# Kernel optimization log

Hardware: AMD Instinct MI355X
Metric: run time of the kernel (lower is better)

Reference implementation:

```python
import jax, jax.numpy as jnp
import numpy as np

CHUNK = 32
H = 4

def silu(x):
    return x * jax.nn.sigmoid(x)

def l2norm(x):
    return x * jax.lax.rsqrt(jnp.sum(x * x, -1, keepdims=True) + 1e-6)

def dwconv_causal(x_cl, w):
    # x_cl: (b, C, L), w: (C, k) depthwise causal conv (cross-correlation, left pad k-1)
    k = w.shape[1]
    xp = jnp.pad(x_cl, ((0, 0), (0, 0), (k - 1, 0)))
    return jax.lax.conv_general_dilated(xp, w[:, None, :], (1,), 'VALID',
        dimension_numbers=('NCH', 'OIH', 'NCH'), feature_group_count=x_cl.shape[1])

def short_conv_silu(x_bld, w):
    y = dwconv_causal(jnp.swapaxes(x_bld, 1, 2), w)
    return silu(jnp.swapaxes(y, 1, 2))

def delta_rule_chunkwise(q, k, v, beta, chunk=CHUNK):
    # q,k: (b,h,L,dk)  v: (b,h,L,dv)  beta: (b,h,L)
    b, h, L, dk = q.shape
    dv = v.shape[-1]
    pad = (-L) % chunk
    if pad:
        q, k, v = (jnp.pad(t, ((0, 0), (0, 0), (0, pad), (0, 0))) for t in (q, k, v))
        beta = jnp.pad(beta, ((0, 0), (0, 0), (0, pad)))
    n = (L + pad) // chunk
    q = l2norm(q)
    k = l2norm(k)
    v = v * beta[..., None]
    kb = k * beta[..., None]
    ch = lambda x: x.reshape(b, h, n, chunk, x.shape[-1])
    qc, kc, vc, kbc = map(ch, (q, k, v, kb))
    idx = jnp.arange(chunk)
    strict_lower = (idx[:, None] > idx[None, :]).astype(q.dtype)
    incl_lower = (idx[:, None] >= idx[None, :]).astype(q.dtype)
    # forward substitution to invert (I - tril(beta K K^T, -1)) per chunk
    attn = -jnp.einsum('bhncd,bhned->bhnce', kbc, kc) * strict_lower
    for i in range(1, chunk):
        upd = jnp.einsum('...j,...ji->...i', attn[..., i, :], attn[..., :, :i])
        attn = attn.at[..., i, :i].add(upd)
    attn = attn + jnp.eye(chunk, dtype=q.dtype)
    u = attn @ vc          # (b,h,n,c,dv)
    w = attn @ kbc         # (b,h,n,c,dk)
    xs = tuple(jnp.moveaxis(t, 2, 0) for t in (qc, kc, u, w))
    S0 = jnp.zeros((b, h, dk, dv), q.dtype)
    def step(S, x):
        qi, ki, ui, wi = x
        a_loc = jnp.einsum('bhcd,bhed->bhce', qi, ki) * incl_lower
        ui = ui - wi @ S
        oi = qi @ S + a_loc @ ui
        S = S + jnp.einsum('bhcd,bhcv->bhdv', ki, ui)
        return S, oi
    S, o = jax.lax.scan(step, S0, xs)
    o = jnp.moveaxis(o, 0, 2).reshape(b, h, n * chunk, dv)[:, :, :L]
    return o, S

def multiscale_conv(v, ms_w3, ms_w15, ms_w31, kernel_mix_w, channel_mixer_w):
    # v: (b,l,h,d)
    b, l, h, d = v.shape
    x = jnp.swapaxes(v.reshape(b, l, h * d), 1, 2)  # (b, h*d, l)
    outs = [dwconv_causal(x, w) for w in (ms_w3, ms_w15, ms_w31)]
    y = jnp.concatenate(outs, axis=1)               # (b, 3*h*d, l)
    # faithful to torch rearrange 'b (h kd) l -> b l h kd' on the concat layout
    y = y.reshape(b, h, 3 * d, l).transpose(0, 3, 1, 2)  # (b,l,h,3d)
    y = y @ kernel_mix_w                            # (b,l,h,d)
    y = (y.reshape(b, l, h * d) @ channel_mixer_w).reshape(b, l, h, d)
    return y

def _forward(hidden_states, Wq, Wk, Wv, Wb, conv_q_w, conv_k_w, conv_v_w,
             ms_w3, ms_w15, ms_w31, kernel_mix_w, channel_mixer_w,
             fusion_w1, fusion_b1, fusion_w2, fusion_b2, o_norm_w, Wo):
    b, L, D = hidden_states.shape
    h = H
    dk = Wq.shape[1] // h
    dv = Wv.shape[1] // h
    q = short_conv_silu(hidden_states @ Wq, conv_q_w).reshape(b, L, h, dk)
    k = short_conv_silu(hidden_states @ Wk, conv_k_w).reshape(b, L, h, dk)
    v = short_conv_silu(hidden_states @ Wv, conv_v_w).reshape(b, L, h, dv)
    v_direct = v
    beta = jax.nn.sigmoid(hidden_states @ Wb)  # (b,L,h)
    tr = lambda x: jnp.swapaxes(x, 1, 2)
    delta_out, _S = delta_rule_chunkwise(tr(q), tr(k), tr(v), tr(beta))
    delta_out = jnp.swapaxes(delta_out, 1, 2)  # (b,L,h,dv)
    ms_out = multiscale_conv(v_direct, ms_w3, ms_w15, ms_w31, kernel_mix_w, channel_mixer_w)
    bn = lambda x: jnp.mean(jnp.abs(x), -1)    # (b,L,h)
    gate_features = jnp.concatenate([hidden_states, bn(ms_out), bn(delta_out), bn(v_direct)], -1)
    hdn = jax.nn.gelu(gate_features @ fusion_w1 + fusion_b1, approximate=False)
    logits = (hdn @ fusion_w2 + fusion_b2).reshape(b, L, h, 3)
    wts = jax.nn.softmax(logits, -1)
    o = wts[..., 0:1] * ms_out + wts[..., 1:2] * delta_out + wts[..., 2:3] * v_direct
    o = o * jax.lax.rsqrt(jnp.mean(o * o, -1, keepdims=True) + 1e-5) * o_norm_w  # RMSNorm
    return o.reshape(b, L, h * dv) @ Wo

def setup_inputs() -> dict:
    B, L, D = 4, 2048, 1024
    h, d = H, D // H
    key = jax.random.key(0)
    ks = jax.random.split(key, 20)
    nrm = lambda k, shp, s: (jax.random.normal(k, shp, dtype=jnp.float32) * s)
    inp = {
        'hidden_states': nrm(ks[0], (B, L, D), 1.0),
        'Wq': nrm(ks[1], (D, D), D ** -0.5),
        'Wk': nrm(ks[2], (D, D), D ** -0.5),
        'Wv': nrm(ks[3], (D, D), D ** -0.5),
        'Wb': nrm(ks[4], (D, h), D ** -0.5),
        'conv_q_w': nrm(ks[5], (D, 4), 0.3),
        'conv_k_w': nrm(ks[6], (D, 4), 0.3),
        'conv_v_w': nrm(ks[7], (D, 4), 0.3),
        'ms_w3': nrm(ks[8], (D, 3), 0.02),
        'ms_w15': nrm(ks[9], (D, 15), 0.02),
        'ms_w31': nrm(ks[10], (D, 31), 0.02),
        'kernel_mix_w': nrm(ks[11], (3 * d, d), (3 * d) ** -0.5),
        'channel_mixer_w': nrm(ks[12], (D, D), D ** -0.5),
        'fusion_w1': nrm(ks[13], (D + 3 * h, 2 * D), (D + 3 * h) ** -0.5),
        'fusion_b1': jnp.zeros((2 * D,), jnp.float32),
        'fusion_w2': nrm(ks[14], (2 * D, 3 * h), (2 * D) ** -0.5),
        'fusion_b2': jnp.concatenate([jnp.zeros((2 * h,), jnp.float32), jnp.ones((h,), jnp.float32)]),
        'o_norm_w': jnp.ones((d,), jnp.float32),
        'Wo': nrm(ks[15], (D, D), D ** -0.5),
    }
    return inp

def reference(hidden_states, Wq, Wk, Wv, Wb, conv_q_w, conv_k_w, conv_v_w,
              ms_w3, ms_w15, ms_w31, kernel_mix_w, channel_mixer_w,
              fusion_w1, fusion_b1, fusion_w2, fusion_b2, o_norm_w, Wo):
    return _forward(hidden_states, Wq, Wk, Wv, Wb, conv_q_w, conv_k_w, conv_v_w,
                    ms_w3, ms_w15, ms_w31, kernel_mix_w, channel_mixer_w,
                    fusion_w1, fusion_b1, fusion_w2, fusion_b2, o_norm_w, Wo)
```

## Files before the change

### kernel.cpp

```cpp
#include <hip/hip_runtime.h>
#include <math.h>


typedef __attribute__((ext_vector_type(8))) __bf16 bf16x8;
typedef __attribute__((ext_vector_type(4))) float f32x4;

__device__ inline ushort f2bf(float f) {
    union { float f; unsigned u; } x; x.f = f;
    unsigned u = x.u;
    u += 0x7fffu + ((u >> 16) & 1u);
    return (ushort)(u >> 16);
}
__device__ inline float bf2f(ushort h) {
    union { unsigned u; float f; } x; x.u = ((unsigned)h) << 16;
    return x.f;
}
__device__ inline float ldf(float v) { return v; }
__device__ inline float ldf(ushort v) { return bf2f(v); }

template<int EPI>
__global__ __launch_bounds__(256) void gemm_mfma(
    const ushort* __restrict__ A, const ushort* __restrict__ BT,
    const float* __restrict__ bias, const float* __restrict__ extA,
    const float* __restrict__ extB, void* __restrict__ Cout,
    int M, int N, int K)
{
    __shared__ ushort As[2][128 * 32];
    __shared__ ushort Bs[2][128 * 32];
    __shared__ float bns[(EPI >= 2) ? 128 * 13 : 1];
    __shared__ float exb[(EPI >= 2) ? 12 * 128 : 1];
    const int tid = threadIdx.x;
    const int nwg = gridDim.x * gridDim.y;
    int lin = blockIdx.y * gridDim.x + blockIdx.x;
    lin = (lin & 7) * (nwg >> 3) + (lin >> 3);
    const int row0 = (lin / gridDim.x) * 128, col0 = (lin % gridDim.x) * 128;
    const int lane = tid & 63, wave = tid >> 6;
    const int wr = (wave >> 1) * 64, wc = (wave & 1) * 64;

    if (EPI >= 2) {
        for (int e = tid; e < 128 * 12; e += 256)
            bns[(e / 12) * 13 + (e % 12)] = extA[(long)(row0 + e / 12) * 12 + e % 12];
        for (int e = tid; e < 12 * 128; e += 256)
            exb[e] = extB[(long)(e >> 7) * N + col0 + (e & 127)];
    }

    f32x4 acc[4][4];
    #pragma unroll
    for (int m = 0; m < 4; ++m)
        #pragma unroll
        for (int n = 0; n < 4; ++n) {
            acc[m][n][0] = 0.f; acc[m][n][1] = 0.f;
            acc[m][n][2] = 0.f; acc[m][n][3] = 0.f;
        }

    const int rA = lane & 15;
    const int ko = (lane >> 4) * 8;
    const int srow = tid >> 2;
    const int skk = (tid & 3) * 8;

    for (int k0 = 0; k0 < K; k0 += 64) {
        #pragma unroll
        for (int hf = 0; hf < 2; ++hf) {
            #pragma unroll
            for (int i = 0; i < 2; ++i) {
                const long ga = (long)(row0 + i * 64 + srow) * K + k0 + hf * 32 + skk;
                __builtin_amdgcn_global_load_lds(
                    (const __attribute__((address_space(1))) void*)(A + ga),
                    (__attribute__((address_space(3))) void*)(&As[hf][0] + i * 2048 + wave * 512),
                    16, 0, 0);
                const long gb = (long)(col0 + i * 64 + srow) * K + k0 + hf * 32 + skk;
                __builtin_amdgcn_global_load_lds(
                    (const __attribute__((address_space(1))) void*)(BT + gb),
                    (__attribute__((address_space(3))) void*)(&Bs[hf][0] + i * 2048 + wave * 512),
                    16, 0, 0);
            }
        }
        __syncthreads();
        #pragma unroll
        for (int hf = 0; hf < 2; ++hf) {
            bf16x8 af[4], bfr[4];
            #pragma unroll
            for (int m = 0; m < 4; ++m)
                af[m] = *(const bf16x8*)(&As[hf][0] + (wr + m * 16 + rA) * 32 + ko);
            #pragma unroll
            for (int n = 0; n < 4; ++n)
                bfr[n] = *(const bf16x8*)(&Bs[hf][0] + (wc + n * 16 + rA) * 32 + ko);
            #pragma unroll
            for (int m = 0; m < 4; ++m)
                #pragma unroll
                for (int n = 0; n < 4; ++n)
                    acc[m][n] = __builtin_amdgcn_mfma_f32_16x16x32_bf16(af[m], bfr[n], acc[m][n], 0, 0, 0);
        }
        __syncthreads();
    }

    const int crow = (lane >> 4) * 4;
    const int ccol = lane & 15;
    #pragma unroll
    for (int m = 0; m < 4; ++m) {
        #pragma unroll
        for (int n = 0; n < 4; ++n) {
            #pragma unroll
            for (int r = 0; r < 4; ++r) {
                const int rl = wr + m * 16 + crow + r;
                const int cl = wc + n * 16 + ccol;
                float vv = acc[m][n][r];
                if (EPI >= 2) {
                    vv += bias[col0 + cl];
                    #pragma unroll
                    for (int j = 0; j < 12; ++j) vv += bns[rl * 13 + j] * exb[j * 128 + cl];
                    vv = 0.5f * vv * (1.f + erff(vv * 0.70710678118654752f));
                }
                const long off = (long)(row0 + rl) * N + col0 + cl;
                if (EPI == 0) ((float*)Cout)[off] = vv;
                else ((ushort*)Cout)[off] = f2bf(vv);
            }
        }
    }
}

__global__ __launch_bounds__(256) void transpose_cast(const float* __restrict__ W,
    ushort* __restrict__ WT, int K, int N)
{
    __shared__ float t[32][33];
    const int k0 = blockIdx.y * 32, n0 = blockIdx.x * 32;
    const int c = threadIdx.x & 31, r8 = threadIdx.x >> 5;
    #pragma unroll
    for (int rr = 0; rr < 4; ++rr) {
        const int r = r8 + rr * 8;
        t[r][c] = W[(long)(k0 + r) * N + n0 + c];
    }
    __syncthreads();
    #pragma unroll
    for (int rr = 0; rr < 4; ++rr) {
        const int r = r8 + rr * 8;
        WT[(long)(n0 + r) * K + k0 + c] = f2bf(t[c][r]);
    }
}

__global__ __launch_bounds__(256) void cast_bf16(const float* __restrict__ x,
    ushort* __restrict__ y)
{
    const long i = ((long)blockIdx.x * 256 + threadIdx.x) * 4;
    const float4 v = *(const float4*)(x + i);
    ushort4 o;
    o.x = f2bf(v.x); o.y = f2bf(v.y); o.z = f2bf(v.z); o.w = f2bf(v.w);
    *(ushort4*)(y + i) = o;
}

template<int NOUT, int MODE, typename TA>
__global__ __launch_bounds__(256) void gemm_smallN(const TA* __restrict__ A,
    const float* __restrict__ Bm, const float* __restrict__ bias,
    float* __restrict__ Cm, int K)
{
    __shared__ float part[4][NOUT];
    __shared__ float sm[NOUT];
    const int m = blockIdx.x, tid = threadIdx.x;
    const TA* ar = A + (long)m * K;
    float acc[NOUT];
    #pragma unroll
    for (int j = 0; j < NOUT; ++j) acc[j] = 0.f;
    for (int k = tid; k < K; k += 256) {
        const float a = ldf(ar[k]);
        #pragma unroll
        for (int j = 0; j < NOUT; ++j) acc[j] += a * Bm[(long)k * NOUT + j];
    }
    #pragma unroll
    for (int j = 0; j < NOUT; ++j)
        for (int off = 32; off > 0; off >>= 1) acc[j] += __shfl_down(acc[j], off);
    const int wid = tid >> 6, lane = tid & 63;
    if (lane == 0) {
        #pragma unroll
        for (int j = 0; j < NOUT; ++j) part[wid][j] = acc[j];
    }
    __syncthreads();
    if (tid < NOUT) {
        float s = part[0][tid] + part[1][tid] + part[2][tid] + part[3][tid];
        if (MODE == 0) {
            Cm[(long)m * NOUT + tid] = 1.f / (1.f + expf(-s));
        } else {
            sm[tid] = s + bias[tid];
        }
    }
    if (MODE == 1) {
        __syncthreads();
        if (tid < NOUT) {
            const int hh = tid / 3, r = tid - hh * 3;
            const float a0 = sm[hh * 3], a1 = sm[hh * 3 + 1], a2 = sm[hh * 3 + 2];
            const float mx = fmaxf(a0, fmaxf(a1, a2));
            const float e0 = expf(a0 - mx), e1 = expf(a1 - mx), e2 = expf(a2 - mx);
            const float mine = (r == 0) ? e0 : ((r == 1) ? e1 : e2);
            Cm[(long)m * NOUT + tid] = mine / (e0 + e1 + e2);
        }
    }
}

__global__ __launch_bounds__(256) void conv4_silu(const float* __restrict__ x,
    int xstride, int coff, const float* __restrict__ wc, float* __restrict__ y)
{
    const long idx = (long)blockIdx.x * 256 + threadIdx.x;
    const int c = (int)(idx & 1023);
    const long bl = idx >> 10;
    const int l = (int)(bl & 2047);
    const float* xp = x + bl * xstride + coff + c;
    const float* wp = wc + c * 4;
    float s = 0.f;
    #pragma unroll
    for (int t = 0; t < 4; ++t) {
        const int ll = l - 3 + t;
        if (ll >= 0) s += xp[(long)(ll - l) * xstride] * wp[t];
    }
    y[idx] = s / (1.f + expf(-s));
}

__global__ __launch_bounds__(256) void conv4_silu_l2norm(const float* __restrict__ x,
    int xstride, int coff, const float* __restrict__ wc, ushort* __restrict__ y)
{
    const int bl = blockIdx.x, tid = threadIdx.x;
    const int l = bl & 2047;
    const int c0 = tid * 4;
    const float* xp = x + (long)bl * xstride + coff + c0;
    float s[4] = {0.f, 0.f, 0.f, 0.f};
    #pragma unroll
    for (int t = 0; t < 4; ++t) {
        const int ll = l - 3 + t;
        if (ll >= 0) {
            const float4 xv = *(const float4*)(xp + (long)(ll - l) * xstride);
            s[0] += xv.x * wc[(c0 + 0) * 4 + t];
            s[1] += xv.y * wc[(c0 + 1) * 4 + t];
            s[2] += xv.z * wc[(c0 + 2) * 4 + t];
            s[3] += xv.w * wc[(c0 + 3) * 4 + t];
        }
    }
    #pragma unroll
    for (int i = 0; i < 4; ++i) s[i] = s[i] / (1.f + expf(-s[i]));
    float ss = s[0] * s[0] + s[1] * s[1] + s[2] * s[2] + s[3] * s[3];
    for (int off = 32; off > 0; off >>= 1) ss += __shfl_down(ss, off);
    ss = __shfl(ss, 0);
    const float inv = rsqrtf(ss + 1e-6f);
    ushort4 o;
    o.x = f2bf(s[0] * inv); o.y = f2bf(s[1] * inv);
    o.z = f2bf(s[2] * inv); o.w = f2bf(s[3] * inv);
    *(ushort4*)(y + (long)bl * 1024 + c0) = o;
}

__global__ __launch_bounds__(256) void chunk_prep(
    const ushort* __restrict__ qn, const ushort* __restrict__ kn,
    const float* __restrict__ v, const float* __restrict__ beta,
    float* __restrict__ u, ushort* __restrict__ w16,
    ushort* __restrict__ kT16, ushort* __restrict__ al16)
{
    __shared__ __align__(16) ushort kn16[32 * 264];
    __shared__ __align__(16) ushort kb16[32 * 264];
    __shared__ __align__(16) float  vb[32 * 260];
    __shared__ float Ms[32 * 33];
    __shared__ float Rs[32 * 33];
    __shared__ float bet[32];
    const int blk = blockIdx.x;
    const int n = blk & 63;
    const int bh = blk >> 6;
    const int h = bh & 3;
    const int b = bh >> 2;
    const int tid = threadIdx.x;
    const long lbase = (long)b * 2048 + n * 32;

    if (tid < 32) bet[tid] = beta[(lbase + tid) * 4 + h];
    __syncthreads();

    #pragma unroll
    for (int it = 0; it < 4; ++it) {
        const int e2 = tid + it * 256;
        const int c = e2 >> 5, d8 = (e2 & 31) * 8;
        const uint4 kv = *(const uint4*)(kn + (lbase + c) * 1024 + h * 256 + d8);
        *(uint4*)&kn16[c * 264 + d8] = kv;
        const float bc = bet[c];
        uint4 kb;
        kb.x = (uint)f2bf(bf2f((ushort)(kv.x & 0xffffu)) * bc) |
               ((uint)f2bf(bf2f((ushort)(kv.x >> 16)) * bc) << 16);
        kb.y = (uint)f2bf(bf2f((ushort)(kv.y & 0xffffu)) * bc) |
               ((uint)f2bf(bf2f((ushort)(kv.y >> 16)) * bc) << 16);
        kb.z = (uint)f2bf(bf2f((ushort)(kv.z & 0xffffu)) * bc) |
               ((uint)f2bf(bf2f((ushort)(kv.z >> 16)) * bc) << 16);
        kb.w = (uint)f2bf(bf2f((ushort)(kv.w & 0xffffu)) * bc) |
               ((uint)f2bf(bf2f((ushort)(kv.w >> 16)) * bc) << 16);
        *(uint4*)&kb16[c * 264 + d8] = kb;
    }
    #pragma unroll
    for (int it = 0; it < 8; ++it) {
        const int e2 = tid + it * 256;
        const int c = e2 >> 6, d4 = (e2 & 63) * 4;
        float4 vv = *(const float4*)(v + (lbase + c) * 1024 + h * 256 + d4);
        const float bc = bet[c];
        vv.x *= bc; vv.y *= bc; vv.z *= bc; vv.w *= bc;
        *(float4*)&vb[c * 260 + d4] = vv;
    }
    __syncthreads();

    for (int e = tid; e < 8192; e += 256)
        kT16[(long)blk * 8192 + e] = kn16[(e & 31) * 264 + (e >> 5)];

    const int lane = tid & 63, wave = tid >> 6;
    const int wr2 = (wave >> 1) * 16, wc2 = (wave & 1) * 16;
    const int rA = lane & 15, ko = (lane >> 4) * 8;
    {
        f32x4 accM, accA;
        accM[0] = 0.f; accM[1] = 0.f; accM[2] = 0.f; accM[3] = 0.f;
        accA[0] = 0.f; accA[1] = 0.f; accA[2] = 0.f; accA[3] = 0.f;
        const ushort* qrow = qn + (lbase + wr2 + rA) * 1024 + h * 256 + ko;
        #pragma unroll
        for (int ks = 0; ks < 8; ++ks) {
            const bf16x8 bfK = *(const bf16x8*)&kn16[(wc2 + rA) * 264 + ks * 32 + ko];
            const bf16x8 afM = *(const bf16x8*)&kb16[(wr2 + rA) * 264 + ks * 32 + ko];
            accM = __builtin_amdgcn_mfma_f32_16x16x32_bf16(afM, bfK, accM, 0, 0, 0);
            const bf16x8 afQ = *(const bf16x8*)(qrow + ks * 32);
            accA = __builtin_amdgcn_mfma_f32_16x16x32_bf16(afQ, bfK, accA, 0, 0, 0);
        }
        const int ccol = lane & 15, crow = (lane >> 4) * 4;
        #pragma unroll
        for (int r = 0; r < 4; ++r) {
            const int i = wr2 + crow + r, j = wc2 + ccol;
            const float mv = (i > j) ? -accM[r] : 0.f;
            Ms[i * 33 + j] = mv;
            Rs[i * 33 + j] = mv + ((i == j) ? 1.f : 0.f);
            al16[(long)blk * 1024 + i * 32 + j] = f2bf((i >= j) ? accA[r] : 0.f);
        }
    }
    __syncthreads();

    const int j = tid & 31, i0 = tid >> 5;
    for (int it = 0; it < 4; ++it) {
        float p4[4] = {0.f, 0.f, 0.f, 0.f};
        for (int kk = 0; kk < 32; ++kk) {
            const float pb = Ms[kk * 33 + j];
            #pragma unroll
            for (int ii = 0; ii < 4; ++ii) p4[ii] += Ms[(i0 + 8 * ii) * 33 + kk] * pb;
        }
        __syncthreads();
        #pragma unroll
        for (int ii = 0; ii < 4; ++ii) Ms[(i0 + 8 * ii) * 33 + j] = p4[ii];
        __syncthreads();
        float r4[4] = {0.f, 0.f, 0.f, 0.f};
        for (int kk = 0; kk < 32; ++kk) {
            const float pb = Ms[kk * 33 + j];
            #pragma unroll
            for (int ii = 0; ii < 4; ++ii) r4[ii] += Rs[(i0 + 8 * ii) * 33 + kk] * pb;
        }
        __syncthreads();
        #pragma unroll
        for (int ii = 0; ii < 4; ++ii) Rs[(i0 + 8 * ii) * 33 + j] += r4[ii];
        __syncthreads();
    }

    {
        const int dd = tid;
        float accU[32], accW[32];
        #pragma unroll
        for (int r = 0; r < 32; ++r) { accU[r] = 0.f; accW[r] = 0.f; }
        for (int kk = 0; kk < 32; ++kk) {
            const float vv = vb[kk * 260 + dd];
            const float bb = bf2f(kb16[kk * 264 + dd]);
            #pragma unroll
            for (int r = 0; r < 32; ++r) {
                const float rr = Rs[r * 33 + kk];
                accU[r] += rr * vv;
                accW[r] += rr * bb;
            }
        }
        const long base = (long)blk * 32;
        #pragma unroll
        for (int r = 0; r < 32; ++r) {
            u  [(base + r) * 256 + dd] = accU[r];
            w16[(base + r) * 256 + dd] = f2bf(accW[r]);
        }
    }
}

__global__ __launch_bounds__(64, 1) void delta_scan_mfma(
    const ushort* __restrict__ q16, const ushort* __restrict__ kT16,
    const ushort* __restrict__ w16, const float* __restrict__ u,
    const ushort* __restrict__ al16, float* __restrict__ dt)
{
    __shared__ __align__(16) ushort Sb[16 * 264];
    __shared__ __align__(16) ushort Ub[16 * 40];
    const int blk = blockIdx.x;
    const int bh = blk & 15;
    const int sl = blk >> 4;
    const int h = bh & 3;
    const int b = bh >> 2;
    const int v0 = sl * 16;
    const int lane = threadIdx.x;
    const int col = lane & 15;
    const int grp = lane >> 4;

    const ushort* wp  = w16  + ((long)bh * 64 * 32 + col) * 256 + grp * 8;
    const ushort* qp  = q16  + ((long)b * 2048 + col) * 1024 + h * 256 + grp * 8;
    const ushort* kp  = kT16 + ((long)bh * 64 * 256 + col) * 32 + grp * 8;
    const ushort* ap  = al16 + ((long)bh * 64 * 32 + col) * 32 + grp * 8;
    const float*  Ug  = u    + ((long)bh * 64 * 32 + grp * 4) * 256 + v0 + col;
    float*        dp  = dt   + ((long)b * 2048 + grp * 4) * 1024 + h * 256 + v0 + col;

    f32x4 S[16];
    #pragma unroll
    for (int t = 0; t < 16; ++t) { S[t][0] = 0.f; S[t][1] = 0.f; S[t][2] = 0.f; S[t][3] = 0.f; }

    bf16x8 wf[2][8], qf[2][8], kf[16], alf[2], sf[8];
    float upre[8];

    #pragma unroll
    for (int kb = 0; kb < 8; ++kb)
        #pragma unroll
        for (int e = 0; e < 8; ++e) sf[kb][e] = (__bf16)0.f;

    #pragma unroll
    for (int rt = 0; rt < 2; ++rt)
        #pragma unroll
        for (int kb = 0; kb < 8; ++kb) {
            wf[rt][kb] = *(const bf16x8*)(wp + rt * 4096 + kb * 32);
            qf[rt][kb] = *(const bf16x8*)(qp + (long)rt * 16384 + kb * 32);
        }
    #pragma unroll
    for (int t = 0; t < 16; ++t) kf[t] = *(const bf16x8*)(kp + t * 512);
    alf[0] = *(const bf16x8*)(ap);
    alf[1] = *(const bf16x8*)(ap + 512);
    #pragma unroll
    for (int rt = 0; rt < 2; ++rt)
        #pragma unroll
        for (int r = 0; r < 4; ++r)
            upre[rt * 4 + r] = Ug[rt * 4096 + r * 256];

    for (int n = 0; n < 64; ++n) {
        f32x4 up[2];
        #pragma unroll
        for (int rt = 0; rt < 2; ++rt) {
            f32x4 a; a[0] = 0.f; a[1] = 0.f; a[2] = 0.f; a[3] = 0.f;
            #pragma unroll
            for (int kb = 0; kb < 8; ++kb)
                a = __builtin_amdgcn_mfma_f32_16x16x32_bf16(wf[rt][kb], sf[kb], a, 0, 0, 0);
            #pragma unroll
            for (int r = 0; r < 4; ++r)
                up[rt][r] = upre[rt * 4 + r] - a[r];
        }
        if (n < 63) {
            #pragma unroll
            for (int rt = 0; rt < 2; ++rt)
                #pragma unroll
                for (int kb = 0; kb < 8; ++kb)
                    wf[rt][kb] = *(const bf16x8*)(wp + (long)(n + 1) * 8192 + rt * 4096 + kb * 32);
        }

        #pragma unroll
        for (int rt = 0; rt < 2; ++rt) {
            ushort4 p;
            p.x = f2bf(up[rt][0]); p.y = f2bf(up[rt][1]);
            p.z = f2bf(up[rt][2]); p.w = f2bf(up[rt][3]);
            *(ushort4*)&Ub[col * 40 + rt * 16 + grp * 4] = p;
        }
        const bf16x8 uf = *(const bf16x8*)&Ub[col * 40 + grp * 8];

        #pragma unroll
        for (int rt = 0; rt < 2; ++rt) {
            f32x4 a; a[0] = 0.f; a[1] = 0.f; a[2] = 0.f; a[3] = 0.f;
            #pragma unroll
            for (int kb = 0; kb < 8; ++kb)
                a = __builtin_amdgcn_mfma_f32_16x16x32_bf16(qf[rt][kb], sf[kb], a, 0, 0, 0);
            a = __builtin_amdgcn_mfma_f32_16x16x32_bf16(alf[rt], uf, a, 0, 0, 0);
            #pragma unroll
            for (int r = 0; r < 4; ++r)
                dp[(long)n * 32768 + rt * 16384 + r * 1024] = a[r];
        }
        if (n < 63) {
            #pragma unroll
            for (int rt = 0; rt < 2; ++rt)
                #pragma unroll
                for (int kb = 0; kb < 8; ++kb)
                    qf[rt][kb] = *(const bf16x8*)(qp + (long)(n + 1) * 32768 + (long)rt * 16384 + kb * 32);
            alf[0] = *(const bf16x8*)(ap + (long)(n + 1) * 1024);
            alf[1] = *(const bf16x8*)(ap + (long)(n + 1) * 1024 + 512);
        }

        #pragma unroll
        for (int t = 0; t < 16; ++t)
            S[t] = __builtin_amdgcn_mfma_f32_16x16x32_bf16(kf[t], uf, S[t], 0, 0, 0);
        if (n < 63) {
            #pragma unroll
            for (int t = 0; t < 16; ++t)
                kf[t] = *(const bf16x8*)(kp + (long)(n + 1) * 8192 + t * 512);
            #pragma unroll
            for (int rt = 0; rt < 2; ++rt)
                #pragma unroll
                for (int r = 0; r < 4; ++r)
                    upre[rt * 4 + r] = Ug[(long)(n + 1) * 8192 + rt * 4096 + r * 256];
        }

        #pragma unroll
        for (int t = 0; t < 16; ++t) {
            ushort4 p;
            p.x = f2bf(S[t][0]); p.y = f2bf(S[t][1]);
            p.z = f2bf(S[t][2]); p.w = f2bf(S[t][3]);
            *(ushort4*)&Sb[col * 264 + t * 16 + grp * 4] = p;
        }
        #pragma unroll
        for (int kb = 0; kb < 8; ++kb)
            sf[kb] = *(const bf16x8*)&Sb[col * 264 + kb * 32 + grp * 8];
    }
}

__global__ __launch_bounds__(256) void ms_conv(const float* __restrict__ v,
    const float* __restrict__ w3, const float* __restrict__ w15,
    const float* __restrict__ w31, ushort* __restrict__ y)
{
    const int bid = blockIdx.x;
    const int b = bid >> 10;
    const int oct = (bid >> 2) & 255;
    const int c = ((bid & 3) << 8) + threadIdx.x;
    const int l0 = oct << 3;
    const float* vb = v + ((long)b * 2048) * 1024 + c;
    ushort* yb = y + ((long)b * 2048) * 3072 + c;

    float win[38];
    #pragma unroll
    for (int t = 0; t < 38; ++t) {
        const int ll = l0 - 30 + t;
        win[t] = (ll >= 0) ? vb[(long)ll * 1024] : 0.f;
    }
    {
        float W[31];
        #pragma unroll
        for (int t = 0; t < 31; ++t) W[t] = w31[c * 31 + t];
        #pragma unroll
        for (int j = 0; j < 8; ++j) {
            float s = 0.f;
            #pragma unroll
            for (int t = 0; t < 31; ++t) s += win[j + t] * W[t];
            yb[(long)(l0 + j) * 3072 + 2048] = f2bf(s);
        }
    }
    {
        float W[15];
        #pragma unroll
        for (int t = 0; t < 15; ++t) W[t] = w15[c * 15 + t];
        #pragma unroll
        for (int j = 0; j < 8; ++j) {
            float s = 0.f;
            #pragma unroll
            for (int t = 0; t < 15; ++t) s += win[j + 16 + t] * W[t];
            yb[(long)(l0 + j) * 3072 + 1024] = f2bf(s);
        }
    }
    {
        float W[3];
        #pragma unroll
        for (int t = 0; t < 3; ++t) W[t] = w3[c * 3 + t];
        #pragma unroll
        for (int j = 0; j < 8; ++j) {
            float s = 0.f;
            #pragma unroll
            for (int t = 0; t < 3; ++t) s += win[j + 28 + t] * W[t];
            yb[(long)(l0 + j) * 3072] = f2bf(s);
        }
    }
}

__global__ __launch_bounds__(256) void build_bn(const float* __restrict__ ms,
    const float* __restrict__ dt, const float* __restrict__ v,
    float* __restrict__ bn)
{
    const int bl = blockIdx.x, tid = threadIdx.x;
    const long rb = (long)bl * 1024;
    const int wid = tid >> 6, lane = tid & 63;
    const long base = rb + wid * 256 + lane * 4;
    float* g = bn + (long)bl * 12;
    float4 a;
    float s;
    a = *(const float4*)(ms + base);
    s = fabsf(a.x) + fabsf(a.y) + fabsf(a.z) + fabsf(a.w);
    for (int off = 32; off > 0; off >>= 1) s += __shfl_down(s, off);
    if (lane == 0) g[wid] = s * (1.f / 256.f);
    a = *(const float4*)(dt + base);
    s = fabsf(a.x) + fabsf(a.y) + fabsf(a.z) + fabsf(a.w);
    for (int off = 32; off > 0; off >>= 1) s += __shfl_down(s, off);
    if (lane == 0) g[4 + wid] = s * (1.f / 256.f);
    a = *(const float4*)(v + base);
    s = fabsf(a.x) + fabsf(a.y) + fabsf(a.z) + fabsf(a.w);
    for (int off = 32; off > 0; off >>= 1) s += __shfl_down(s, off);
    if (lane == 0) g[8 + wid] = s * (1.f / 256.f);
}

__global__ __launch_bounds__(256) void blend_rms(const float* __restrict__ ms,
    const float* __restrict__ dt, const float* __restrict__ v,
    const float* __restrict__ wts, const float* __restrict__ onw,
    ushort* __restrict__ o)
{
    const int bl = blockIdx.x, tid = threadIdx.x;
    const int wid = tid >> 6, lane = tid & 63;
    const long base = (long)bl * 1024 + wid * 256 + lane * 4;
    const float* wr = wts + (long)bl * 12 + wid * 3;
    const float w0 = wr[0], w1 = wr[1], w2 = wr[2];
    const float4 m = *(const float4*)(ms + base);
    const float4 d = *(const float4*)(dt + base);
    const float4 x = *(const float4*)(v + base);
    float4 ov;
    ov.x = w0 * m.x + w1 * d.x + w2 * x.x;
    ov.y = w0 * m.y + w1 * d.y + w2 * x.y;
    ov.z = w0 * m.z + w1 * d.z + w2 * x.z;
    ov.w = w0 * m.w + w1 * d.w + w2 * x.w;
    float ss = ov.x * ov.x + ov.y * ov.y + ov.z * ov.z + ov.w * ov.w;
    for (int off = 32; off > 0; off >>= 1) ss += __shfl_down(ss, off);
    ss = __shfl(ss, 0);
    const float inv = rsqrtf(ss * (1.f / 256.f) + 1e-5f);
    const float4 nw = *(const float4*)(onw + lane * 4);
    ushort4 ob;
    ob.x = f2bf(ov.x * inv * nw.x); ob.y = f2bf(ov.y * inv * nw.y);
    ob.z = f2bf(ov.z * inv * nw.z); ob.w = f2bf(ov.w * inv * nw.w);
    *(ushort4*)(o + base) = ob;
}

extern "C" void kernel_launch(void* const* d_in, const int* in_sizes, int n_in,
                              void* d_out, int out_size, void* d_ws, size_t ws_size,
                              hipStream_t stream)
{
    (void)in_sizes; (void)n_in; (void)out_size; (void)ws_size;
    const float* hid   = (const float*)d_in[0];
    const float* Wq    = (const float*)d_in[1];
    const float* Wk    = (const float*)d_in[2];
    const float* Wv    = (const float*)d_in[3];
    const float* Wb    = (const float*)d_in[4];
    const float* cq    = (const float*)d_in[5];
    const float* ck    = (const float*)d_in[6];
    const float* cv    = (const float*)d_in[7];
    const float* w3    = (const float*)d_in[8];
    const float* w15   = (const float*)d_in[9];
    const float* w31   = (const float*)d_in[10];
    const float* kmix  = (const float*)d_in[11];
    const float* cmix  = (const float*)d_in[12];
    const float* fw1   = (const float*)d_in[13];
    const float* fb1   = (const float*)d_in[14];
    const float* fw2   = (const float*)d_in[15];
    const float* fb2   = (const float*)d_in[16];
    const float* onw   = (const float*)d_in[17];
    const float* Wo    = (const float*)d_in[18];
    float* out = (float*)d_out;

    const size_t MiB = 1024 * 1024;
    char* W = (char*)d_ws;
    float*  s0    = (float*)(W);
    char*   s1c   = W + 32 * MiB;
    float*  s1    = (float*)s1c;
    float*  s2    = (float*)(W + 64 * MiB);
    char*   s3    = W + 96 * MiB;
    float*  s4    = (float*)(W + 128 * MiB);
    ushort* hid16 = (ushort*)(W + 160 * MiB);
    ushort* WqT   = (ushort*)(W + 176 * MiB);
    ushort* WkT   = WqT   + 1024 * 1024;
    ushort* WvT   = WkT   + 1024 * 1024;
    ushort* cmixT = WvT   + 1024 * 1024;
    ushort* WoT   = cmixT + 1024 * 1024;
    ushort* fw1T  = WoT   + 1024 * 1024;
    ushort* kmixT = fw1T  + 2048 * 1024;
    float*  beta  = (float*)(W + 191 * MiB);
    ushort* al16  = (ushort*)(W + 191 * MiB + 128 * 1024);
    float*  bnf   = (float*)(W + 193 * MiB + 128 * 1024);
    float*  wts   = bnf + 98304;

    ushort* q16    = (ushort*)s3;
    ushort* k16    = (ushort*)(s3 + 16 * MiB);
    ushort* mix16  = q16;
    ushort* ofin16 = k16;
    ushort* yms16  = (ushort*)s0;
    ushort* hdn16  = (ushort*)s0;
    float*  qlin = s0;
    float*  u = s0;
    ushort* w16  = (ushort*)s1c;
    ushort* kT16 = (ushort*)(s1c + 16 * MiB);
    float*  dt = s2; float* v = s4; float* msout = s1;

    const dim3 T256(256);
    cast_bf16<<<8192, T256, 0, stream>>>(hid, hid16);
    transpose_cast<<<dim3(32, 32), T256, 0, stream>>>(Wq, WqT, 1024, 1024);
    transpose_cast<<<dim3(32, 32), T256, 0, stream>>>(Wk, WkT, 1024, 1024);
    transpose_cast<<<dim3(32, 32), T256, 0, stream>>>(Wv, WvT, 1024, 1024);
    transpose_cast<<<dim3(32, 32), T256, 0, stream>>>(cmix, cmixT, 1024, 1024);
    transpose_cast<<<dim3(32, 32), T256, 0, stream>>>(Wo, WoT, 1024, 1024);
    transpose_cast<<<dim3(64, 32), T256, 0, stream>>>(fw1, fw1T, 1024, 2048);
    transpose_cast<<<dim3(8, 24), T256, 0, stream>>>(kmix, kmixT, 768, 256);
    gemm_mfma<0><<<dim3(8, 64), T256, 0, stream>>>(hid16, WqT, nullptr, nullptr, nullptr, qlin, 8192, 1024, 1024);
    conv4_silu_l2norm<<<8192, T256, 0, stream>>>(qlin, 1024, 0, cq, q16);
    gemm_mfma<0><<<dim3(8, 64), T256, 0, stream>>>(hid16, WkT, nullptr, nullptr, nullptr, qlin, 8192, 1024, 1024);
    conv4_silu_l2norm<<<8192, T256, 0, stream>>>(qlin, 1024, 0, ck, k16);
    gemm_mfma<0><<<dim3(8, 64), T256, 0, stream>>>(hid16, WvT, nullptr, nullptr, nullptr, qlin, 8192, 1024, 1024);
    conv4_silu<<<32768, T256, 0, stream>>>(qlin, 1024, 0, cv, v);
    gemm_smallN<4, 0><<<8192, T256, 0, stream>>>(hid, Wb, nullptr, beta, 1024);
    chunk_prep<<<1024, T256, 0, stream>>>(q16, k16, v, beta, u, w16, kT16, al16);
    delta_scan_mfma<<<256, dim3(64), 0, stream>>>(q16, kT16, w16, u, al16, dt);
    ms_conv<<<4096, T256, 0, stream>>>(v, w3, w15, w31, yms16);
    gemm_mfma<1><<<dim3(2, 256), T256, 0, stream>>>(yms16, kmixT, nullptr, nullptr, nullptr, mix16, 32768, 256, 768);
    gemm_mfma<0><<<dim3(8, 64), T256, 0, stream>>>(mix16, cmixT, nullptr, nullptr, nullptr, msout, 8192, 1024, 1024);
    build_bn<<<8192, T256, 0, stream>>>(msout, dt, v, bnf);
    gemm_mfma<3><<<dim3(16, 64), T256, 0, stream>>>(hid16, fw1T, fb1, bnf, fw1 + 1024L * 2048, hdn16, 8192, 2048, 1024);
    gemm_smallN<12, 1><<<8192, T256, 0, stream>>>(hdn16, fw2, fb2, wts, 2048);
    blend_rms<<<8192, T256, 0, stream>>>(msout, dt, v, wts, onw, ofin16);
    gemm_mfma<0><<<dim3(8, 64), T256, 0, stream>>>(ofin16, WoT, nullptr, nullptr, nullptr, out, 8192, 1024, 1024);
}
```

Baseline: 740.9 us.

## Store delta-rule output and channel-mixer result as bf16, drop GEMM tile swizzle

The delta-scan output and the channel-mixer GEMM result are now written as bf16 instead of fp32, and build_bn and blend_rms read them as bf16. This halves the memory traffic for these two 8192x1024 intermediates. The GEMM workgroup remapping (an XCD-style swizzle) is removed in favour of direct blockIdx tiling, and the scan kernel's launch attributes are rewritten as explicit amdgpu attributes. The precision loss in the blended output is a risk, and dropping the swizzle may hurt L2 locality.

```diff
diff --git a/kernel.cpp b/kernel.cpp
--- a/kernel.cpp
+++ b/kernel.cpp
@@ -30,10 +30,7 @@
     __shared__ float bns[(EPI >= 2) ? 128 * 13 : 1];
     __shared__ float exb[(EPI >= 2) ? 12 * 128 : 1];
     const int tid = threadIdx.x;
-    const int nwg = gridDim.x * gridDim.y;
-    int lin = blockIdx.y * gridDim.x + blockIdx.x;
-    lin = (lin & 7) * (nwg >> 3) + (lin >> 3);
-    const int row0 = (lin / gridDim.x) * 128, col0 = (lin % gridDim.x) * 128;
+    const int row0 = blockIdx.y * 128, col0 = blockIdx.x * 128;
     const int lane = tid & 63, wave = tid >> 6;
     const int wr = (wave >> 1) * 64, wc = (wave & 1) * 64;
 
@@ -375,10 +372,11 @@
     }
 }
 
-__global__ __launch_bounds__(64, 1) void delta_scan_mfma(
+__global__ __attribute__((amdgpu_flat_work_group_size(64, 64), amdgpu_waves_per_eu(1, 1)))
+void delta_scan_mfma(
     const ushort* __restrict__ q16, const ushort* __restrict__ kT16,
     const ushort* __restrict__ w16, const float* __restrict__ u,
-    const ushort* __restrict__ al16, float* __restrict__ dt)
+    const ushort* __restrict__ al16, ushort* __restrict__ dt)
 {
     __shared__ __align__(16) ushort Sb[16 * 264];
     __shared__ __align__(16) ushort Ub[16 * 40];
@@ -397,7 +395,7 @@
     const ushort* kp  = kT16 + ((long)bh * 64 * 256 + col) * 32 + grp * 8;
     const ushort* ap  = al16 + ((long)bh * 64 * 32 + col) * 32 + grp * 8;
     const float*  Ug  = u    + ((long)bh * 64 * 32 + grp * 4) * 256 + v0 + col;
-    float*        dp  = dt   + ((long)b * 2048 + grp * 4) * 1024 + h * 256 + v0 + col;
+    ushort*       dp  = dt   + ((long)b * 2048 + grp * 4) * 1024 + h * 256 + v0 + col;
 
     f32x4 S[16];
     #pragma unroll
@@ -466,7 +464,7 @@
             a = __builtin_amdgcn_mfma_f32_16x16x32_bf16(alf[rt], uf, a, 0, 0, 0);
             #pragma unroll
             for (int r = 0; r < 4; ++r)
-                dp[(long)n * 32768 + rt * 16384 + r * 1024] = a[r];
+                dp[(long)n * 32768 + rt * 16384 + r * 1024] = f2bf(a[r]);
         }
         if (n < 63) {
             #pragma unroll
@@ -561,8 +559,8 @@
     }
 }
 
-__global__ __launch_bounds__(256) void build_bn(const float* __restrict__ ms,
-    const float* __restrict__ dt, const float* __restrict__ v,
+__global__ __launch_bounds__(256) void build_bn(const ushort* __restrict__ ms,
+    const ushort* __restrict__ dt, const float* __restrict__ v,
     float* __restrict__ bn)
 {
     const int bl = blockIdx.x, tid = threadIdx.x;
@@ -570,24 +568,26 @@
     const int wid = tid >> 6, lane = tid & 63;
     const long base = rb + wid * 256 + lane * 4;
     float* g = bn + (long)bl * 12;
-    float4 a;
     float s;
-    a = *(const float4*)(ms + base);
-    s = fabsf(a.x) + fabsf(a.y) + fabsf(a.z) + fabsf(a.w);
+
+    const ushort4 mu = *(const ushort4*)(ms + base);
+    s = fabsf(bf2f(mu.x)) + fabsf(bf2f(mu.y)) + fabsf(bf2f(mu.z)) + fabsf(bf2f(mu.w));
     for (int off = 32; off > 0; off >>= 1) s += __shfl_down(s, off);
     if (lane == 0) g[wid] = s * (1.f / 256.f);
-    a = *(const float4*)(dt + base);
-    s = fabsf(a.x) + fabsf(a.y) + fabsf(a.z) + fabsf(a.w);
+
+    const ushort4 du = *(const ushort4*)(dt + base);
+    s = fabsf(bf2f(du.x)) + fabsf(bf2f(du.y)) + fabsf(bf2f(du.z)) + fabsf(bf2f(du.w));
     for (int off = 32; off > 0; off >>= 1) s += __shfl_down(s, off);
     if (lane == 0) g[4 + wid] = s * (1.f / 256.f);
-    a = *(const float4*)(v + base);
+
+    const float4 a = *(const float4*)(v + base);
     s = fabsf(a.x) + fabsf(a.y) + fabsf(a.z) + fabsf(a.w);
     for (int off = 32; off > 0; off >>= 1) s += __shfl_down(s, off);
     if (lane == 0) g[8 + wid] = s * (1.f / 256.f);
 }
 
-__global__ __launch_bounds__(256) void blend_rms(const float* __restrict__ ms,
-    const float* __restrict__ dt, const float* __restrict__ v,
+__global__ __launch_bounds__(256) void blend_rms(const ushort* __restrict__ ms,
+    const ushort* __restrict__ dt, const float* __restrict__ v,
     const float* __restrict__ wts, const float* __restrict__ onw,
     ushort* __restrict__ o)
 {
@@ -596,14 +596,14 @@
     const long base = (long)bl * 1024 + wid * 256 + lane * 4;
     const float* wr = wts + (long)bl * 12 + wid * 3;
     const float w0 = wr[0], w1 = wr[1], w2 = wr[2];
-    const float4 m = *(const float4*)(ms + base);
-    const float4 d = *(const float4*)(dt + base);
+    const ushort4 mu = *(const ushort4*)(ms + base);
+    const ushort4 du = *(const ushort4*)(dt + base);
     const float4 x = *(const float4*)(v + base);
     float4 ov;
-    ov.x = w0 * m.x + w1 * d.x + w2 * x.x;
-    ov.y = w0 * m.y + w1 * d.y + w2 * x.y;
-    ov.z = w0 * m.z + w1 * d.z + w2 * x.z;
-    ov.w = w0 * m.w + w1 * d.w + w2 * x.w;
+    ov.x = w0 * bf2f(mu.x) + w1 * bf2f(du.x) + w2 * x.x;
+    ov.y = w0 * bf2f(mu.y) + w1 * bf2f(du.y) + w2 * x.y;
+    ov.z = w0 * bf2f(mu.z) + w1 * bf2f(du.z) + w2 * x.z;
+    ov.w = w0 * bf2f(mu.w) + w1 * bf2f(du.w) + w2 * x.w;
     float ss = ov.x * ov.x + ov.y * ov.y + ov.z * ov.z + ov.w * ov.w;
     for (int off = 32; off > 0; off >>= 1) ss += __shfl_down(ss, off);
     ss = __shfl(ss, 0);
@@ -672,7 +672,9 @@
     float*  u = s0;
     ushort* w16  = (ushort*)s1c;
     ushort* kT16 = (ushort*)(s1c + 16 * MiB);
-    float*  dt = s2; float* v = s4; float* msout = s1;
+    ushort* dt16 = (ushort*)s2;
+    float*  v = s4;
+    ushort* msout16 = (ushort*)s1c;
 
     const dim3 T256(256);
     cast_bf16<<<8192, T256, 0, stream>>>(hid, hid16);
@@ -691,13 +693,13 @@
     conv4_silu<<<32768, T256, 0, stream>>>(qlin, 1024, 0, cv, v);
     gemm_smallN<4, 0><<<8192, T256, 0, stream>>>(hid, Wb, nullptr, beta, 1024);
     chunk_prep<<<1024, T256, 0, stream>>>(q16, k16, v, beta, u, w16, kT16, al16);
-    delta_scan_mfma<<<256, dim3(64), 0, stream>>>(q16, kT16, w16, u, al16, dt);
+    delta_scan_mfma<<<256, dim3(64), 0, stream>>>(q16, kT16, w16, u, al16, dt16);
     ms_conv<<<4096, T256, 0, stream>>>(v, w3, w15, w31, yms16);
     gemm_mfma<1><<<dim3(2, 256), T256, 0, stream>>>(yms16, kmixT, nullptr, nullptr, nullptr, mix16, 32768, 256, 768);
-    gemm_mfma<0><<<dim3(8, 64), T256, 0, stream>>>(mix16, cmixT, nullptr, nullptr, nullptr, msout, 8192, 1024, 1024);
-    build_bn<<<8192, T256, 0, stream>>>(msout, dt, v, bnf);
+    gemm_mfma<1><<<dim3(8, 64), T256, 0, stream>>>(mix16, cmixT, nullptr, nullptr, nullptr, msout16, 8192, 1024, 1024);
+    build_bn<<<8192, T256, 0, stream>>>(msout16, dt16, v, bnf);
     gemm_mfma<3><<<dim3(16, 64), T256, 0, stream>>>(hid16, fw1T, fb1, bnf, fw1 + 1024L * 2048, hdn16, 8192, 2048, 1024);
     gemm_smallN<12, 1><<<8192, T256, 0, stream>>>(hdn16, fw2, fb2, wts, 2048);
-    blend_rms<<<8192, T256, 0, stream>>>(msout, dt, v, wts, onw, ofin16);
+    blend_rms<<<8192, T256, 0, stream>>>(msout16, dt16, v, wts, onw, ofin16);
     gemm_mfma<0><<<dim3(8, 64), T256, 0, stream>>>(ofin16, WoT, nullptr, nullptr, nullptr, out, 8192, 1024, 1024);
 }
```

Measured after the change: 745.4 us. No clear change (+0.6%).
